# Optimization experiments

Hardware: AMD Instinct MI355X
Metric: run time of the kernel (lower is better)

Reference implementation:

```python
import jax, jax.numpy as jnp
import numpy as np

N = 100000      # num_nodes
FEAT = 256      # num_features
H = 128         # hidden
C = 40          # num_classes
K = 4           # hops
RWS = 10        # random-walk samples per node
NL = 2          # nlayer
ALPHA = 0.1


def setup_inputs() -> dict:
    key = jax.random.key(0)
    ks = jax.random.split(key, 10)
    x = jax.random.normal(ks[0], (N, FEAT), dtype=jnp.float32)
    degree = jax.random.uniform(ks[1], (N,), minval=1.0, maxval=64.0, dtype=jnp.float32)
    # precomputed random-walk endpoints per layer per hop: [NL, K, N*RWS]
    ends = jax.random.randint(ks[2], (NL, K, N * RWS), 0, N, dtype=jnp.int32)
    # att init: alpha*(1-alpha)^k, last entry (1-alpha)^K, tiled per layer
    a = ALPHA * (1.0 - ALPHA) ** jnp.arange(K + 1, dtype=jnp.float32)
    a = a.at[-1].set((1.0 - ALPHA) ** K)
    att = jnp.tile(a[None, :], (NL, 1))
    def lin(k, fan_in, fan_out):
        s = 1.0 / np.sqrt(fan_in)
        return jax.random.uniform(k, (fan_in, fan_out), minval=-s, maxval=s, dtype=jnp.float32)
    W0 = lin(ks[3], FEAT, H)
    b0 = jnp.zeros((H,), dtype=jnp.float32)
    W1 = lin(ks[4], H, H)
    b1 = jnp.zeros((H,), dtype=jnp.float32)
    W2 = lin(ks[5], H, C)
    b2 = jnp.zeros((C,), dtype=jnp.float32)
    return {"x": x, "degree": degree, "ends": ends, "att": att,
            "W0": W0, "b0": b0, "W1": W1, "b1": b1, "W2": W2, "b2": b2}


def reference(x, degree, ends, att, W0, b0, W1, b1, W2, b2):
    Ws = [(W0, b0), (W1, b1)]
    starts = jnp.repeat(jnp.arange(N), RWS)          # [N*RWS] walk start node ids
    d_sqrt = jnp.sqrt(degree)                        # degree^0.5
    d_isqrt = jax.lax.rsqrt(degree)                  # degree^-0.5
    h = x
    for i in range(NL):
        W, b = Ws[i]
        h = h @ W + b                                # Linear (dropout p=0)
        mask = att[i]                                # [K+1]
        agg = h * mask[0]
        for k in range(1, K + 1):
            e = ends[i, k - 1]                       # [N*RWS] hop-k endpoints
            w = d_sqrt[starts] * d_isqrt[e]          # degree reweighting
            samp = (w[:, None] * h[e]).reshape(N, RWS, h.shape[1]).mean(axis=1)
            agg = agg + samp * mask[k]
        h = jax.nn.relu(agg)
    logits = h @ W2 + b2
    return jax.nn.log_softmax(logits, axis=1)
```

## Files before the change

kernel.cpp:

```cpp
#include <hip/hip_runtime.h>
#include <math.h>

#define NNODES 100000
#define NFEAT  256
#define HID    128
#define NCLS   40
#define KHOP   4
#define RWSAMP 10
#define KP1    5

typedef __bf16 bf16;
typedef __attribute__((ext_vector_type(8)))  __bf16 bf16x8;
typedef __attribute__((ext_vector_type(2)))  float  f32x2;
typedef __attribute__((ext_vector_type(16))) float  f32x16;

__global__ __launch_bounds__(256) void prep_w(
    const float* __restrict__ W0, const float* __restrict__ W1,
    const float* __restrict__ W2,
    bf16* __restrict__ Wt0, bf16* __restrict__ Wt1, bf16* __restrict__ Wt2)
{
    int tid = blockIdx.x * 256 + threadIdx.x;
    if (tid < 128 * 256) {
        int n = tid >> 8, k = tid & 255;
        Wt0[tid] = (bf16)W0[k * 128 + n];
    } else if (tid < 128 * 256 + 128 * 128) {
        int i = tid - 128 * 256;
        int n = i >> 7, k = i & 127;
        Wt1[i] = (bf16)W1[k * 128 + n];
    } else if (tid < 128 * 256 + 128 * 128 + 64 * 128) {
        int i = tid - (128 * 256 + 128 * 128);
        int n = i >> 7, k = i & 127;
        Wt2[i] = (n < NCLS) ? (bf16)W2[k * NCLS + n] : (bf16)0.0f;
    }
}

template<int K, bool A_BF16>
__global__ __launch_bounds__(256) void gemm_nodes(
    const void* __restrict__ Av, const bf16* __restrict__ Wt,
    const float* __restrict__ bias, const float* __restrict__ degree,
    unsigned char* __restrict__ F8, int M)
{
    constexpr int BK  = 128;
    constexpr int LDB = BK + 4;
    __shared__ bf16 Bs[128 * LDB];
    __shared__ bf16 As[4][32 * LDB];

    const int tid  = threadIdx.x;
    const int wv   = tid >> 6;
    const int lane = tid & 63;
    const int l31  = lane & 31;
    const int lhi  = lane >> 5;
    const int blockRow = blockIdx.x * 128;
    const int rowBase  = blockRow + wv * 32;

    const bf16*  Ab = (const bf16*)Av;
    const float* Af = (const float*)Av;

    f32x16 acc[4];
#pragma unroll
    for (int t = 0; t < 4; ++t)
#pragma unroll
        for (int r = 0; r < 16; ++r) acc[t][r] = 0.0f;

    for (int k0 = 0; k0 < K; k0 += BK) {
        if (k0) __syncthreads();
#pragma unroll 4
        for (int l = 0; l < 8; ++l) {
            int c   = tid + l * 256;
            int row = c >> 4;
            int kc  = (c & 15) * 8;
            uint4 v = *(const uint4*)(Wt + (size_t)row * K + k0 + kc);
            *(uint2*)&Bs[row * LDB + kc]     = make_uint2(v.x, v.y);
            *(uint2*)&Bs[row * LDB + kc + 4] = make_uint2(v.z, v.w);
        }
        __syncthreads();

        if (A_BF16) {
#pragma unroll 4
            for (int l = 0; l < 8; ++l) {
                int c  = lane + l * 64;
                int r  = c >> 4;
                int kc = (c & 15) * 8;
                int gr = min(rowBase + r, M - 1);
                uint4 v = *(const uint4*)(Ab + (size_t)gr * K + k0 + kc);
                *(uint2*)&As[wv][r * LDB + kc]     = make_uint2(v.x, v.y);
                *(uint2*)&As[wv][r * LDB + kc + 4] = make_uint2(v.z, v.w);
            }
        } else {
#pragma unroll 4
            for (int l = 0; l < 16; ++l) {
                int c  = lane + l * 64;
                int r  = c >> 5;
                int kc = (c & 31) * 4;
                int gr = min(rowBase + r, M - 1);
                float4 v = *(const float4*)(Af + (size_t)gr * K + k0 + kc);
                union { bf16 h[4]; uint2 u; } t4;
                t4.h[0] = (bf16)v.x; t4.h[1] = (bf16)v.y;
                t4.h[2] = (bf16)v.z; t4.h[3] = (bf16)v.w;
                *(uint2*)&As[wv][r * LDB + kc] = t4.u;
            }
        }

#pragma unroll
        for (int ks = 0; ks < BK / 16; ++ks) {
            const int ko = ks * 16 + lhi * 8;
            union { uint2 u2[2]; bf16x8 v; } ua, ub;
            ua.u2[0] = *(const uint2*)&As[wv][l31 * LDB + ko];
            ua.u2[1] = *(const uint2*)&As[wv][l31 * LDB + ko + 4];
            bf16x8 a = ua.v;
#pragma unroll
            for (int t = 0; t < 4; ++t) {
                ub.u2[0] = *(const uint2*)&Bs[(t * 32 + l31) * LDB + ko];
                ub.u2[1] = *(const uint2*)&Bs[(t * 32 + l31) * LDB + ko + 4];
                acc[t] = __builtin_amdgcn_mfma_f32_32x32x16_bf16(a, ub.v, acc[t], 0, 0, 0);
            }
        }
    }

    float rsd[16];
#pragma unroll
    for (int G = 0; G < 4; ++G) {
        int r0 = blockRow + 4 * (wv * 8 + 2 * G + lhi);
#pragma unroll
        for (int c = 0; c < 4; ++c)
            rsd[4 * G + c] = rsqrtf(degree[min(r0 + c, M - 1)]);
    }

    __syncthreads();
    unsigned* ldsq = (unsigned*)Bs;

#pragma unroll
    for (int t = 0; t < 4; ++t) {
        int col = t * 32 + l31;
        float bc = bias[col];
#pragma unroll
        for (int G = 0; G < 4; ++G) {
            float v0 = (acc[t][4 * G + 0] + bc) * rsd[4 * G + 0];
            float v1 = (acc[t][4 * G + 1] + bc) * rsd[4 * G + 1];
            float v2 = (acc[t][4 * G + 2] + bc) * rsd[4 * G + 2];
            float v3 = (acc[t][4 * G + 3] + bc) * rsd[4 * G + 3];
            int p = __builtin_amdgcn_cvt_pk_fp8_f32(v0, v1, 0, false);
            p = __builtin_amdgcn_cvt_pk_fp8_f32(v2, v3, p, true);
            ldsq[(wv * 8 + 2 * G + lhi) * 128 + col] = (unsigned)p;
        }
    }
    __syncthreads();

    {
        const int j  = tid & 31;
        const int Q0 = (tid >> 5) * 4;
#pragma unroll
        for (int qq = 0; qq < 4; ++qq) {
            int Q = Q0 + qq;
            uint4 d = *(const uint4*)&ldsq[Q * 128 + 4 * j];
            int growb = blockRow + 4 * Q;
#pragma unroll
            for (int i = 0; i < 4; ++i) {
                unsigned sel = ((unsigned)(4 + i) << 8) | (unsigned)i;
                unsigned lo = __builtin_amdgcn_perm(d.y, d.x, sel);
                unsigned hi = __builtin_amdgcn_perm(d.w, d.z, sel);
                unsigned o  = __builtin_amdgcn_perm(hi, lo, 0x05040100u);
                if (growb + i < M)
                    *(unsigned*)(F8 + (size_t)(growb + i) * 128 + 4 * j) = o;
            }
        }
    }
}

__global__ __launch_bounds__(256) void agg_relu_fp8(
    const unsigned char* __restrict__ hf8, bf16* __restrict__ hout,
    const int* __restrict__ ends, const float* __restrict__ degree,
    const float* __restrict__ att)
{
    __shared__ int   sewE[4][2][40];
    __shared__ float sw[44];

    const int wv   = threadIdx.x >> 6;
    const int lane = threadIdx.x & 63;
    const int n0   = blockIdx.x * 8 + wv * 2;

    if (threadIdx.x < 44) {
        int j = threadIdx.x;
        float w;
        if (j < 40)       w = att[j / RWSAMP + 1] * (1.0f / RWSAMP);
        else if (j == 40) w = att[0];
        else              w = 0.0f;
        sw[j] = w;
    }

    for (int en = lane; en < 80; en += 64) {
        int which = en >= 40;
        int l = en - which * 40;
        int n = n0 + which;
        int k = l / RWSAMP, s = l - k * RWSAMP;
        int e = ends[(size_t)k * (NNODES * RWSAMP) + (size_t)n * RWSAMP + s];
        sewE[wv][which][l] = e << 7;
    }
    __syncthreads();

    const int q  = lane >> 4;
    const int c8 = (lane & 15) * 8;

    f32x2 a0[4], a1[4];
#pragma unroll
    for (int i = 0; i < 4; ++i) { a0[i] = (f32x2){0.f, 0.f}; a1[i] = (f32x2){0.f, 0.f}; }

#pragma unroll
    for (int t = 0; t < 11; ++t) {
        int j = 4 * t + q;
        int e0, e1;
        if (t < 10) { e0 = sewE[wv][0][j]; e1 = sewE[wv][1][j]; }
        else        { e0 = n0 << 7;        e1 = (n0 + 1) << 7; }
        float w = sw[j];
        uint2 g0 = *(const uint2*)(hf8 + (unsigned)e0 + (unsigned)c8);
        uint2 g1 = *(const uint2*)(hf8 + (unsigned)e1 + (unsigned)c8);
        f32x2 w2 = {w, w};
        a0[0] = __builtin_elementwise_fma(w2, __builtin_amdgcn_cvt_pk_f32_fp8((int)g0.x, false), a0[0]);
        a0[1] = __builtin_elementwise_fma(w2, __builtin_amdgcn_cvt_pk_f32_fp8((int)g0.x, true),  a0[1]);
        a0[2] = __builtin_elementwise_fma(w2, __builtin_amdgcn_cvt_pk_f32_fp8((int)g0.y, false), a0[2]);
        a0[3] = __builtin_elementwise_fma(w2, __builtin_amdgcn_cvt_pk_f32_fp8((int)g0.y, true),  a0[3]);
        a1[0] = __builtin_elementwise_fma(w2, __builtin_amdgcn_cvt_pk_f32_fp8((int)g1.x, false), a1[0]);
        a1[1] = __builtin_elementwise_fma(w2, __builtin_amdgcn_cvt_pk_f32_fp8((int)g1.x, true),  a1[1]);
        a1[2] = __builtin_elementwise_fma(w2, __builtin_amdgcn_cvt_pk_f32_fp8((int)g1.y, false), a1[2]);
        a1[3] = __builtin_elementwise_fma(w2, __builtin_amdgcn_cvt_pk_f32_fp8((int)g1.y, true),  a1[3]);
    }

#pragma unroll
    for (int i = 0; i < 4; ++i) {
        a0[i].x += __shfl_xor(a0[i].x, 16, 64); a0[i].y += __shfl_xor(a0[i].y, 16, 64);
        a1[i].x += __shfl_xor(a1[i].x, 16, 64); a1[i].y += __shfl_xor(a1[i].y, 16, 64);
        a0[i].x += __shfl_xor(a0[i].x, 32, 64); a0[i].y += __shfl_xor(a0[i].y, 32, 64);
        a1[i].x += __shfl_xor(a1[i].x, 32, 64); a1[i].y += __shfl_xor(a1[i].y, 32, 64);
    }

    if (q < 2) {
        const int n = n0 + q;
        f32x2* a = (q == 0) ? a0 : a1;
        float sd = sqrtf(degree[n]);
        f32x2 sd2 = {sd, sd}, z = {0.f, 0.f};
#pragma unroll
        for (int i = 0; i < 4; ++i) {
            a[i] = __builtin_elementwise_max(a[i], z);
            a[i] = a[i] * sd2;
        }

        union { bf16 h[8]; uint4 u; } st;
        st.h[0] = (bf16)a[0].x; st.h[1] = (bf16)a[0].y;
        st.h[2] = (bf16)a[1].x; st.h[3] = (bf16)a[1].y;
        st.h[4] = (bf16)a[2].x; st.h[5] = (bf16)a[2].y;
        st.h[6] = (bf16)a[3].x; st.h[7] = (bf16)a[3].y;
        *(uint4*)(hout + (size_t)n * HID + c8) = st.u;
    }
}

__global__ __launch_bounds__(256) void head_mfma(
    const bf16* __restrict__ h, const bf16* __restrict__ Wt2,
    const float* __restrict__ b2, float* __restrict__ out, int M)
{
    constexpr int K = HID, LDB = K + 8;
    __shared__ bf16 Bs[64 * LDB];

    const int tid = threadIdx.x;
    constexpr int CPR = K / 8;
    for (int f = tid; f < 64 * CPR; f += 256) {
        int row = f / CPR;
        int kc  = (f % CPR) * 8;
        *(uint4*)&Bs[row * LDB + kc] = *(const uint4*)(Wt2 + (size_t)row * K + kc);
    }
    __syncthreads();

    const int wv   = tid >> 6;
    const int lane = tid & 63;
    const int l31  = lane & 31;
    const int lhi  = lane >> 5;
    const int blockRow = blockIdx.x * 128;
    const int arow = min(blockRow + wv * 32 + l31, M - 1);

    f32x16 acc[2];
#pragma unroll
    for (int t = 0; t < 2; ++t)
#pragma unroll
        for (int r = 0; r < 16; ++r) acc[t][r] = 0.0f;

#pragma unroll
    for (int ks = 0; ks < K / 16; ++ks) {
        bf16x8 a = *(const bf16x8*)(h + (size_t)arow * K + ks * 16 + lhi * 8);
#pragma unroll
        for (int t = 0; t < 2; ++t) {
            bf16x8 b = *(const bf16x8*)&Bs[(t * 32 + l31) * LDB + ks * 16 + lhi * 8];
            acc[t] = __builtin_amdgcn_mfma_f32_32x32x16_bf16(a, b, acc[t], 0, 0, 0);
        }
    }

    const float bc0 = b2[l31];
    const float bc1 = (l31 < 8) ? b2[32 + l31] : 0.0f;

#pragma unroll
    for (int r = 0; r < 16; ++r) {
        float v0 = acc[0][r] + bc0;
        float v1 = (l31 < 8) ? (acc[1][r] + bc1) : -INFINITY;

        float m = fmaxf(v0, v1);
#pragma unroll
        for (int off = 16; off > 0; off >>= 1)
            m = fmaxf(m, __shfl_xor(m, off, 64));

        float s = __expf(v0 - m) + ((l31 < 8) ? __expf(v1 - m) : 0.0f);
#pragma unroll
        for (int off = 16; off > 0; off >>= 1)
            s += __shfl_xor(s, off, 64);

        float ls = __logf(s);
        int grow = blockRow + wv * 32 + (r & 3) + 8 * (r >> 2) + 4 * lhi;
        if (grow < M) {
            out[(size_t)grow * NCLS + l31] = v0 - m - ls;
            if (l31 < 8)
                out[(size_t)grow * NCLS + 32 + l31] = v1 - m - ls;
        }
    }
}

extern "C" void kernel_launch(void* const* d_in, const int* in_sizes, int n_in,
                              void* d_out, int out_size, void* d_ws, size_t ws_size,
                              hipStream_t stream)
{
    const float* x      = (const float*)d_in[0];
    const float* degree = (const float*)d_in[1];
    const int*   ends   = (const int*)  d_in[2];
    const float* att    = (const float*)d_in[3];
    const float* W0     = (const float*)d_in[4];
    const float* b0     = (const float*)d_in[5];
    const float* W1     = (const float*)d_in[6];
    const float* b1     = (const float*)d_in[7];
    const float* W2     = (const float*)d_in[8];
    const float* b2     = (const float*)d_in[9];
    float* out = (float*)d_out;

    bf16* hb0 = (bf16*)d_ws;
    bf16* hb1 = hb0 + (size_t)NNODES * HID;
    unsigned char* hf8 = (unsigned char*)(hb1 + (size_t)NNODES * HID);
    bf16* Wt0 = (bf16*)(hf8 + (size_t)NNODES * HID);
    bf16* Wt1 = Wt0 + 128 * 256;
    bf16* Wt2 = Wt1 + 128 * 128;

    const int prepN = 128 * 256 + 128 * 128 + 64 * 128;
    prep_w<<<(prepN + 255) / 256, 256, 0, stream>>>(W0, W1, W2, Wt0, Wt1, Wt2);

    const int gGemm = (NNODES + 127) / 128;
    const int gAgg  = (NNODES + 7) / 8;

    gemm_nodes<NFEAT, false><<<gGemm, 256, 0, stream>>>(x, Wt0, b0, degree, hf8, NNODES);
    agg_relu_fp8<<<gAgg, 256, 0, stream>>>(hf8, hb1, ends, degree, att);
    gemm_nodes<HID, true><<<gGemm, 256, 0, stream>>>(hb1, Wt1, b1, degree, hf8, NNODES);
    agg_relu_fp8<<<gAgg, 256, 0, stream>>>(
        hf8, hb0, ends + (size_t)KHOP * NNODES * RWSAMP, degree, att + KP1);
    head_mfma<<<gGemm, 256, 0, stream>>>(hb0, Wt2, b2, out, NNODES);
}
```

Measured before the change: 334.7 us.

## Split fp8 feature table into column slices to shrink gather working set

The GEMM epilogue now writes the fp8 hidden features as two column-sliced tables (64 bytes per node each), and the aggregation kernel is launched over twice as many blocks, each handling one slice. Each slice table is 6.4 MB instead of 12.8 MB, so random-walk gathers within a slice hit a smaller footprint that fits better in L2/MALL. Lane mapping changes so 8 lanes cover one 64-byte row and 8 sample groups run in parallel. The cost is reading the ends indices and degrees twice and launching double the blocks. The self term is weighted only in one lane group so it is added once.

Result: slower. 368.1 us (+10.0%).

```diff
diff --git a/kernel.cpp b/kernel.cpp
--- a/kernel.cpp
+++ b/kernel.cpp
@@ -8,6 +8,10 @@
 #define KHOP   4
 #define RWSAMP 10
 #define KP1    5
+
+#define NSLICE 2
+#define SLB    64
+#define NBAGG  ((NNODES + 7) / 8)
 
 typedef __bf16 bf16;
 typedef __attribute__((ext_vector_type(8)))  __bf16 bf16x8;
@@ -149,6 +153,8 @@
     {
         const int j  = tid & 31;
         const int Q0 = (tid >> 5) * 4;
+        const int slice = j >> 4;
+        const int b4    = (j & 15) * 4;
 #pragma unroll
         for (int qq = 0; qq < 4; ++qq) {
             int Q = Q0 + qq;
@@ -161,23 +167,26 @@
                 unsigned hi = __builtin_amdgcn_perm(d.w, d.z, sel);
                 unsigned o  = __builtin_amdgcn_perm(hi, lo, 0x05040100u);
                 if (growb + i < M)
-                    *(unsigned*)(F8 + (size_t)(growb + i) * 128 + 4 * j) = o;
+                    *(unsigned*)(F8 + ((size_t)slice * NNODES + (growb + i)) * SLB + b4) = o;
             }
         }
     }
 }
 
 __global__ __launch_bounds__(256) void agg_relu_fp8(
-    const unsigned char* __restrict__ hf8, bf16* __restrict__ hout,
+    const unsigned char* __restrict__ hf8s,
+    bf16* __restrict__ hout,
     const int* __restrict__ ends, const float* __restrict__ degree,
     const float* __restrict__ att)
 {
     __shared__ int   sewE[4][2][40];
     __shared__ float sw[44];
 
-    const int wv   = threadIdx.x >> 6;
-    const int lane = threadIdx.x & 63;
-    const int n0   = blockIdx.x * 8 + wv * 2;
+    const int slice = blockIdx.x / NBAGG;
+    const int nb    = blockIdx.x - slice * NBAGG;
+    const int wv    = threadIdx.x >> 6;
+    const int lane  = threadIdx.x & 63;
+    const int n0    = nb * 8 + wv * 2;
 
     if (threadIdx.x < 44) {
         int j = threadIdx.x;
@@ -194,48 +203,45 @@
         int n = n0 + which;
         int k = l / RWSAMP, s = l - k * RWSAMP;
         int e = ends[(size_t)k * (NNODES * RWSAMP) + (size_t)n * RWSAMP + s];
-        sewE[wv][which][l] = e << 7;
+        sewE[wv][which][l] = e << 6;
     }
     __syncthreads();
 
-    const int q  = lane >> 4;
-    const int c8 = (lane & 15) * 8;
-
-    f32x2 a0[4], a1[4];
-#pragma unroll
-    for (int i = 0; i < 4; ++i) { a0[i] = (f32x2){0.f, 0.f}; a1[i] = (f32x2){0.f, 0.f}; }
+    const unsigned char* sbase = hf8s + (size_t)slice * ((size_t)NNODES * SLB);
+
+    const int g    = lane >> 3;
+    const int il   = lane & 7;
+    const int node = g & 1;
+    const int wq   = g >> 1;
+    const int c8   = il * 8;
+
+    f32x2 a[4];
+#pragma unroll
+    for (int i = 0; i < 4; ++i) a[i] = (f32x2){0.f, 0.f};
 
 #pragma unroll
     for (int t = 0; t < 11; ++t) {
-        int j = 4 * t + q;
-        int e0, e1;
-        if (t < 10) { e0 = sewE[wv][0][j]; e1 = sewE[wv][1][j]; }
-        else        { e0 = n0 << 7;        e1 = (n0 + 1) << 7; }
-        float w = sw[j];
-        uint2 g0 = *(const uint2*)(hf8 + (unsigned)e0 + (unsigned)c8);
-        uint2 g1 = *(const uint2*)(hf8 + (unsigned)e1 + (unsigned)c8);
+        int j = 4 * t + wq;
+        int eo;
+        float w;
+        if (t < 10) { eo = sewE[wv][node][j]; w = sw[j]; }
+        else        { eo = (n0 + node) << 6;  w = (wq == 0) ? sw[40] : 0.0f; }
+        uint2 gch = *(const uint2*)(sbase + (unsigned)eo + (unsigned)c8);
         f32x2 w2 = {w, w};
-        a0[0] = __builtin_elementwise_fma(w2, __builtin_amdgcn_cvt_pk_f32_fp8((int)g0.x, false), a0[0]);
-        a0[1] = __builtin_elementwise_fma(w2, __builtin_amdgcn_cvt_pk_f32_fp8((int)g0.x, true),  a0[1]);
-        a0[2] = __builtin_elementwise_fma(w2, __builtin_amdgcn_cvt_pk_f32_fp8((int)g0.y, false), a0[2]);
-        a0[3] = __builtin_elementwise_fma(w2, __builtin_amdgcn_cvt_pk_f32_fp8((int)g0.y, true),  a0[3]);
-        a1[0] = __builtin_elementwise_fma(w2, __builtin_amdgcn_cvt_pk_f32_fp8((int)g1.x, false), a1[0]);
-        a1[1] = __builtin_elementwise_fma(w2, __builtin_amdgcn_cvt_pk_f32_fp8((int)g1.x, true),  a1[1]);
-        a1[2] = __builtin_elementwise_fma(w2, __builtin_amdgcn_cvt_pk_f32_fp8((int)g1.y, false), a1[2]);
-        a1[3] = __builtin_elementwise_fma(w2, __builtin_amdgcn_cvt_pk_f32_fp8((int)g1.y, true),  a1[3]);
+        a[0] = __builtin_elementwise_fma(w2, __builtin_amdgcn_cvt_pk_f32_fp8((int)gch.x, false), a[0]);
+        a[1] = __builtin_elementwise_fma(w2, __builtin_amdgcn_cvt_pk_f32_fp8((int)gch.x, true),  a[1]);
+        a[2] = __builtin_elementwise_fma(w2, __builtin_amdgcn_cvt_pk_f32_fp8((int)gch.y, false), a[2]);
+        a[3] = __builtin_elementwise_fma(w2, __builtin_amdgcn_cvt_pk_f32_fp8((int)gch.y, true),  a[3]);
     }
 
 #pragma unroll
     for (int i = 0; i < 4; ++i) {
-        a0[i].x += __shfl_xor(a0[i].x, 16, 64); a0[i].y += __shfl_xor(a0[i].y, 16, 64);
-        a1[i].x += __shfl_xor(a1[i].x, 16, 64); a1[i].y += __shfl_xor(a1[i].y, 16, 64);
-        a0[i].x += __shfl_xor(a0[i].x, 32, 64); a0[i].y += __shfl_xor(a0[i].y, 32, 64);
-        a1[i].x += __shfl_xor(a1[i].x, 32, 64); a1[i].y += __shfl_xor(a1[i].y, 32, 64);
-    }
-
-    if (q < 2) {
-        const int n = n0 + q;
-        f32x2* a = (q == 0) ? a0 : a1;
+        a[i].x += __shfl_xor(a[i].x, 16, 64); a[i].y += __shfl_xor(a[i].y, 16, 64);
+        a[i].x += __shfl_xor(a[i].x, 32, 64); a[i].y += __shfl_xor(a[i].y, 32, 64);
+    }
+
+    if (lane < 16) {
+        const int n = n0 + (lane >> 3);
         float sd = sqrtf(degree[n]);
         f32x2 sd2 = {sd, sd}, z = {0.f, 0.f};
 #pragma unroll
@@ -243,13 +249,12 @@
             a[i] = __builtin_elementwise_max(a[i], z);
             a[i] = a[i] * sd2;
         }
-
         union { bf16 h[8]; uint4 u; } st;
         st.h[0] = (bf16)a[0].x; st.h[1] = (bf16)a[0].y;
         st.h[2] = (bf16)a[1].x; st.h[3] = (bf16)a[1].y;
         st.h[4] = (bf16)a[2].x; st.h[5] = (bf16)a[2].y;
         st.h[6] = (bf16)a[3].x; st.h[7] = (bf16)a[3].y;
-        *(uint4*)(hout + (size_t)n * HID + c8) = st.u;
+        *(uint4*)(hout + (size_t)n * HID + slice * SLB + c8) = st.u;
     }
 }
 
@@ -347,7 +352,7 @@
     prep_w<<<(prepN + 255) / 256, 256, 0, stream>>>(W0, W1, W2, Wt0, Wt1, Wt2);
 
     const int gGemm = (NNODES + 127) / 128;
-    const int gAgg  = (NNODES + 7) / 8;
+    const int gAgg  = NSLICE * NBAGG;
 
     gemm_nodes<NFEAT, false><<<gGemm, 256, 0, stream>>>(x, Wt0, b0, degree, hf8, NNODES);
     agg_relu_fp8<<<gAgg, 256, 0, stream>>>(hf8, hb1, ends, degree, att);
```
